# Kernel tuning notes

Measured on AMD Instinct MI355X. Metric: run time of the kernel, lower is better.

Reference implementation:

```python
import jax, jax.numpy as jnp
import numpy as np

BN_EPS = 1e-5

SOBEL_X = jnp.array([[-1., 0., 1.], [-2., 0., 2.], [-1., 0., 1.]], jnp.float32).reshape(1, 1, 3, 3)
SOBEL_Y = jnp.array([[-1., -2., -1.], [0., 0., 0.], [1., 2., 1.]], jnp.float32).reshape(1, 1, 3, 3)


def _conv2d(x, w, stride, pad):
    return jax.lax.conv_general_dilated(x, w, window_strides=(stride, stride),
                                        padding=((pad, pad), (pad, pad)),
                                        dimension_numbers=('NCHW', 'OIHW', 'NCHW'))


def _resize_bilinear_align_corners(x, H, W):
    # x: [b,c,h1,w1] -> [b,c,H,W], align_corners=True
    b, c, h1, w1 = x.shape
    ys = jnp.linspace(0., h1 - 1., H)
    xs = jnp.linspace(0., w1 - 1., W)
    y0 = jnp.floor(ys).astype(jnp.int32)
    x0 = jnp.floor(xs).astype(jnp.int32)
    y1 = jnp.minimum(y0 + 1, h1 - 1)
    x1 = jnp.minimum(x0 + 1, w1 - 1)
    wy = (ys - y0)[None, None, :, None]
    wx = (xs - x0)[None, None, None, :]
    top = x[:, :, y0, :]
    bot = x[:, :, y1, :]
    top = top[:, :, :, x0] * (1. - wx) + top[:, :, :, x1] * wx
    bot = bot[:, :, :, x0] * (1. - wx) + bot[:, :, :, x1] * wx
    return top * (1. - wy) + bot * wy


def setup_inputs() -> dict:
    key = jax.random.key(0)
    ks = jax.random.split(key, 6)
    b, c, h, w = 4, 64, 128, 128
    return {
        'x': jax.random.normal(ks[0], (b, c, h, w), jnp.float32),
        'conv_w': jax.random.normal(ks[1], (c, c, 3, 3), jnp.float32) * 0.05,
        'conv_b': jax.random.normal(ks[2], (c,), jnp.float32) * 0.05,
        'bn_gamma': jnp.ones((c,), jnp.float32),
        'bn_beta': jnp.zeros((c,), jnp.float32),
        'bn_mean': jnp.zeros((c,), jnp.float32),
        'bn_var': jnp.ones((c,), jnp.float32),
        'fc1_w': jax.random.normal(ks[3], (c, c), jnp.float32) * 0.1,
        'fc2_w': jax.random.normal(ks[4], (c, c), jnp.float32) * 0.1,
        'fc3_w': jax.random.normal(ks[5], (c, c), jnp.float32) * 0.1,
    }


def reference(x, conv_w, conv_b, bn_gamma, bn_beta, bn_mean, bn_var, fc1_w, fc2_w, fc3_w):
    b, c, h, w = x.shape
    # input block: conv s2 + BN (eval) + relu
    y = _conv2d(x, conv_w, 2, 1) + conv_b[None, :, None, None]
    y = (y - bn_mean[None, :, None, None]) * jax.lax.rsqrt(bn_var + BN_EPS)[None, :, None, None]
    y = jax.nn.relu(y * bn_gamma[None, :, None, None] + bn_beta[None, :, None, None])
    b, c, h1, w1 = y.shape
    N = h1 * w1
    # pre: [b,c,h1,w1] -> [b,1,N,c]
    xp = y.reshape(b, c, N).transpose(0, 2, 1).reshape(b, 1, N, c)
    # Sobel adjacency over the N "node" axis
    sx = jnp.abs(_conv2d(xp, SOBEL_X, 1, 1)).reshape(b, N, c)
    sy = jnp.abs(_conv2d(xp, SOBEL_Y, 1, 1)).reshape(b, N, c)
    A = jnp.einsum('bnc,bmc->bnm', sx, sy)  # [b,N,N]
    # torch nn.Softmax() (no dim) on a 3D tensor => legacy dim=0 (batch axis)
    A = jax.nn.softmax(A, axis=0)
    # normalize: D^-0.5 (A + I) D^-0.5, batched
    A1 = A + jnp.eye(N, dtype=A.dtype)[None]
    dinv = A1.sum(axis=2) ** -0.5  # [b,N]
    A = dinv[:, :, None] * A1 * dinv[:, None, :]
    # GCN propagation; Conv1d k=1 no-bias == channel matmul
    xg = xp.reshape(b, N, c)
    xg = jax.nn.relu(jnp.einsum('bnm,bmc,oc->bno', A, xg, fc1_w))
    xg = jax.nn.relu(jnp.einsum('bnm,bmc,oc->bno', A, xg, fc2_w))
    xg = jnp.einsum('bnm,bmc,oc->bon', A, xg, fc3_w)  # [b,c,N]
    out = xg.reshape(b, c, h1, w1)
    return _resize_bilinear_align_corners(out, h, w)
```

## Files before the change

kernel.cpp:

```cpp
#include <hip/hip_runtime.h>
#include <hip/hip_bf16.h>

typedef float f32x4 __attribute__((ext_vector_type(4)));
typedef short bf16x8 __attribute__((ext_vector_type(8)));

#define NB 4
#define NC 64
#define NH 128
#define NW 128
#define NN 4096
#define BN_EPS_C 1e-5f

__device__ __forceinline__ void gld16(const void* g, void* l) {
    __builtin_amdgcn_global_load_lds((const __attribute__((address_space(1))) void*)g,
                                     (__attribute__((address_space(3))) void*)l, 16, 0, 0);
}
__device__ __forceinline__ ushort pkbf(float f) {
    __hip_bfloat16 h = __float2bfloat16(f);
    return *(ushort*)&h;
}

__global__ __launch_bounds__(256) void k_conv(
    const float* __restrict__ x, const float* __restrict__ cw, const float* __restrict__ cb,
    const float* __restrict__ bng, const float* __restrict__ bnb, const float* __restrict__ bnm,
    const float* __restrict__ bnv, float* __restrict__ xg)
{
    int b = blockIdx.y, oh = blockIdx.x;
    int tid = threadIdx.x;
    int ow = tid & 63;
    int wg = __builtin_amdgcn_readfirstlane(tid >> 6);
    float acc[16];
#pragma unroll
    for (int j = 0; j < 16; ++j) acc[j] = 0.f;
    const float* xb = x + (size_t)b * NC * NH * NW;
    int ih0 = 2 * oh - 1;
    for (int ic = 0; ic < 64; ++ic) {
        const float* xr = xb + (size_t)ic * (NH * NW);
        float v00, v01, v02, v10, v11, v12, v20, v21, v22;
        if (ih0 < 0) { v00 = v01 = v02 = 0.f; }
        else {
            const float* p = xr + ih0 * NW + 2 * ow;
            float2 t = *(const float2*)p;
            v01 = t.x; v02 = t.y;
            v00 = (ow == 0) ? 0.f : p[-1];
        }
        { const float* p = xr + (ih0 + 1) * NW + 2 * ow; float2 t = *(const float2*)p; v11 = t.x; v12 = t.y; v10 = (ow == 0) ? 0.f : p[-1]; }
        { const float* p = xr + (ih0 + 2) * NW + 2 * ow; float2 t = *(const float2*)p; v21 = t.x; v22 = t.y; v20 = (ow == 0) ? 0.f : p[-1]; }
        const float* wp = cw + ((size_t)(wg * 16) * 64 + ic) * 9;
#pragma unroll
        for (int j = 0; j < 16; ++j) {
            const float* wj = wp + (size_t)j * 576;
            acc[j] += wj[0] * v00 + wj[1] * v01 + wj[2] * v02
                    + wj[3] * v10 + wj[4] * v11 + wj[5] * v12
                    + wj[6] * v20 + wj[7] * v21 + wj[8] * v22;
        }
    }
    int n = oh * 64 + ow;
    float* outr = xg + ((size_t)b * NN + n) * 64;
#pragma unroll
    for (int j = 0; j < 16; ++j) {
        int oc = wg * 16 + j;
        float s = bng[oc] * rsqrtf(bnv[oc] + BN_EPS_C);
        float y = (acc[j] + cb[oc] - bnm[oc]) * s + bnb[oc];
        outr[oc] = fmaxf(y, 0.f);
    }
}

__global__ __launch_bounds__(256) void k_sobel(
    const float* __restrict__ xg,
    __hip_bfloat16* __restrict__ xh, __hip_bfloat16* __restrict__ xl,
    __hip_bfloat16* __restrict__ yh, __hip_bfloat16* __restrict__ yl)
{
    __shared__ float t[66][66];
    int b = blockIdx.y;
    int n0 = blockIdx.x * 64;
    int tid = threadIdx.x;
    const float* xb = xg + (size_t)b * NN * 64;
    for (int idx = tid; idx < 66 * 64; idx += 256) {
        int r = idx >> 6, c = idx & 63;
        int n = n0 - 1 + r;
        float v = (n >= 0 && n < NN) ? xb[(size_t)n * 64 + c] : 0.f;
        t[r][c + 1] = v;
    }
    for (int idx = tid; idx < 66; idx += 256) { t[idx][0] = 0.f; t[idx][65] = 0.f; }
    __syncthreads();
    int c = tid & 63, rg = tid >> 6;
    int lc = c + 1;
    for (int i = 0; i < 16; ++i) {
        int r = rg * 16 + i;
        float tm1 = t[r][lc - 1],     t0 = t[r][lc],     tp1 = t[r][lc + 1];
        float mm1 = t[r + 1][lc - 1],                    mp1 = t[r + 1][lc + 1];
        float bm1 = t[r + 2][lc - 1], b0 = t[r + 2][lc], bp1 = t[r + 2][lc + 1];
        float gx = (tp1 + 2.f * mp1 + bp1) - (tm1 + 2.f * mm1 + bm1);
        float gy = (bm1 + 2.f * b0 + bp1) - (tm1 + 2.f * t0 + tp1);
        float ax = fabsf(gx), ay = fabsf(gy);
        size_t o = ((size_t)b * NN + n0 + r) * 64 + c;
        __hip_bfloat16 h1 = __float2bfloat16(ax);
        xh[o] = h1;
        xl[o] = __float2bfloat16(ax - __bfloat162float(h1));
        __hip_bfloat16 h2 = __float2bfloat16(ay);
        yh[o] = h2;
        yl[o] = __float2bfloat16(ay - __bfloat162float(h2));
    }
}

__global__ __launch_bounds__(256) void k_logits(
    const __hip_bfloat16* __restrict__ xh_, const __hip_bfloat16* __restrict__ xl_,
    const __hip_bfloat16* __restrict__ yh_, const __hip_bfloat16* __restrict__ yl_,
    __hip_bfloat16* __restrict__ A, float* __restrict__ rowsum)
{
    __shared__ __align__(16) ushort lds_u[24576];
    ushort* a_hi = lds_u;
    ushort* a_lo = lds_u + 4096;
    ushort* b_hi = lds_u + 8192;
    ushort* b_lo = lds_u + 16384;
    ushort* st   = lds_u;

    const ushort* xh = (const ushort*)xh_;
    const ushort* xl = (const ushort*)xl_;
    const ushort* yh = (const ushort*)yh_;
    const ushort* yl = (const ushort*)yl_;
    int tid = threadIdx.x, lane = tid & 63;
    int w = __builtin_amdgcn_readfirstlane(tid >> 6);
    int l15 = lane & 15, lg = lane >> 4;
    int wn = w >> 1, wm = w & 1;
    int m0 = blockIdx.x * 128, n0 = blockIdx.y * 64;

    f32x4 acc[4][2][4];
#pragma unroll
    for (int b = 0; b < 4; ++b)
#pragma unroll
        for (int t = 0; t < 2; ++t)
#pragma unroll
            for (int u = 0; u < 4; ++u) acc[b][t][u] = (f32x4){0.f, 0.f, 0.f, 0.f};

    for (int b = 0; b < 4; ++b) {
        if (b) __syncthreads();
#pragma unroll
        for (int p = 0; p < 2; ++p) {
            int ch = p * 256 + tid;
            int r = ch >> 3;
            int sc = ((ch & 7) ^ (r & 7)) * 8;
            gld16(xh + ((size_t)b * NN + n0 + r) * 64 + sc, (char*)a_hi + ch * 16);
            gld16(xl + ((size_t)b * NN + n0 + r) * 64 + sc, (char*)a_lo + ch * 16);
        }
#pragma unroll
        for (int p = 0; p < 4; ++p) {
            int ch = p * 256 + tid;
            int r = ch >> 3;
            int sc = ((ch & 7) ^ (r & 7)) * 8;
            gld16(yh + ((size_t)b * NN + m0 + r) * 64 + sc, (char*)b_hi + ch * 16);
            gld16(yl + ((size_t)b * NN + m0 + r) * 64 + sc, (char*)b_lo + ch * 16);
        }
        __syncthreads();
#pragma unroll
        for (int ks = 0; ks < 2; ++ks) {
            bf16x8 ah[2], al2[2], bh4[4], bl4[4];
#pragma unroll
            for (int t = 0; t < 2; ++t) {
                int r = wn * 32 + t * 16 + l15;
                int c16 = (ks * 4 + lg) ^ (r & 7);
                ah[t]  = *(const bf16x8*)((const char*)a_hi + r * 128 + c16 * 16);
                al2[t] = *(const bf16x8*)((const char*)a_lo + r * 128 + c16 * 16);
            }
#pragma unroll
            for (int u = 0; u < 4; ++u) {
                int r = wm * 64 + u * 16 + l15;
                int c16 = (ks * 4 + lg) ^ (r & 7);
                bh4[u] = *(const bf16x8*)((const char*)b_hi + r * 128 + c16 * 16);
                bl4[u] = *(const bf16x8*)((const char*)b_lo + r * 128 + c16 * 16);
            }
#pragma unroll
            for (int t = 0; t < 2; ++t)
#pragma unroll
                for (int u = 0; u < 4; ++u) {
                    f32x4 a = acc[b][t][u];
                    a = __builtin_amdgcn_mfma_f32_16x16x32_bf16(ah[t],  bh4[u], a, 0, 0, 0);
                    a = __builtin_amdgcn_mfma_f32_16x16x32_bf16(ah[t],  bl4[u], a, 0, 0, 0);
                    a = __builtin_amdgcn_mfma_f32_16x16x32_bf16(al2[t], bh4[u], a, 0, 0, 0);
                    acc[b][t][u] = a;
                }
        }
    }

    float rs[4][2][4];
#pragma unroll
    for (int b = 0; b < 4; ++b)
#pragma unroll
        for (int t = 0; t < 2; ++t)
#pragma unroll
            for (int j = 0; j < 4; ++j) rs[b][t][j] = 0.f;
#pragma unroll
    for (int t = 0; t < 2; ++t)
#pragma unroll
        for (int u = 0; u < 4; ++u)
#pragma unroll
            for (int j = 0; j < 4; ++j) {
                float v0 = acc[0][t][u][j], v1 = acc[1][t][u][j];
                float v2 = acc[2][t][u][j], v3 = acc[3][t][u][j];
                float mx = fmaxf(fmaxf(v0, v1), fmaxf(v2, v3));
                float e0 = __expf(v0 - mx), e1 = __expf(v1 - mx);
                float e2 = __expf(v2 - mx), e3 = __expf(v3 - mx);
                float rz = 1.f / (e0 + e1 + e2 + e3);
                acc[0][t][u][j] = e0 * rz; acc[1][t][u][j] = e1 * rz;
                acc[2][t][u][j] = e2 * rz; acc[3][t][u][j] = e3 * rz;
                rs[0][t][j] += e0 * rz; rs[1][t][j] += e1 * rz;
                rs[2][t][j] += e2 * rz; rs[3][t][j] += e3 * rz;
            }
#pragma unroll
    for (int b = 0; b < 4; ++b)
#pragma unroll
        for (int t = 0; t < 2; ++t)
#pragma unroll
            for (int j = 0; j < 4; ++j) {
                float s = rs[b][t][j];
                s += __shfl_xor(s, 1); s += __shfl_xor(s, 2);
                s += __shfl_xor(s, 4); s += __shfl_xor(s, 8);
                if (l15 == 0)
                    atomicAdd(&rowsum[(size_t)b * NN + n0 + wn * 32 + t * 16 + lg * 4 + j], s);
            }

#pragma unroll
    for (int b = 0; b < 4; ++b) {
        __syncthreads();
#pragma unroll
        for (int t = 0; t < 2; ++t)
#pragma unroll
            for (int u = 0; u < 4; ++u)
#pragma unroll
                for (int j = 0; j < 4; ++j) {
                    int row = wn * 32 + t * 16 + lg * 4 + j;
                    int col = wm * 64 + u * 16 + l15;
                    int c16 = (col >> 3) ^ (row & 7);
                    st[row * 128 + c16 * 8 + (col & 7)] = pkbf(acc[b][t][u][j]);
                }
        __syncthreads();
#pragma unroll
        for (int p = 0; p < 4; ++p) {
            int idx = p * 256 + tid;
            int row = idx >> 4, cl = idx & 15;
            int c16 = cl ^ (row & 7);
            bf16x8 v = *(const bf16x8*)(st + row * 128 + c16 * 8);
            *(bf16x8*)((ushort*)A + (size_t)b * NN * NN + (size_t)(n0 + row) * NN + m0 + cl * 8) = v;
        }
    }
}

__global__ __launch_bounds__(256) void k_dinv(const float* __restrict__ rs, float* __restrict__ dinv)
{
    int i = blockIdx.x * 256 + threadIdx.x;
    dinv[i] = rsqrtf(rs[i] + 1.0f);
}

__global__ __launch_bounds__(256) void k_small(
    const float* __restrict__ h, const float* __restrict__ fc, const float* __restrict__ dinv,
    __hip_bfloat16* __restrict__ tT, float* __restrict__ tf)
{
    int blk = blockIdx.x;
    int b = blk >> 6, m0 = (blk & 63) * 64;
    int tid = threadIdx.x;
    int mi = tid & 63, m = m0 + mi;
    int oq = __builtin_amdgcn_readfirstlane(tid >> 6);
    const float* hr = h + ((size_t)b * NN + m) * 64;
    float hv[64];
#pragma unroll
    for (int i = 0; i < 16; ++i) {
        float4 v = *(const float4*)(hr + 4 * i);
        hv[4 * i] = v.x; hv[4 * i + 1] = v.y; hv[4 * i + 2] = v.z; hv[4 * i + 3] = v.w;
    }
    float dv = dinv[(size_t)b * NN + m];
#pragma unroll
    for (int j = 0; j < 16; ++j) {
        int o = oq * 16 + j;
        const float* wr = fc + (size_t)o * 64;
        float a = 0.f;
#pragma unroll
        for (int c2 = 0; c2 < 64; ++c2) a += hv[c2] * wr[c2];
        a *= dv;
        tf[((size_t)b * NN + m) * 64 + o] = a;
        tT[((size_t)b * 64 + o) * NN + m] = __float2bfloat16(a);
    }
}

__global__ __launch_bounds__(256) void k_big(
    const __hip_bfloat16* __restrict__ A_, const __hip_bfloat16* __restrict__ tT_,
    float* __restrict__ part)
{
    __shared__ __align__(16) ushort ab[2][4096];
    const ushort* A = (const ushort*)A_;
    const ushort* tT = (const ushort*)tT_;
    int blk = blockIdx.x;
    int ntile = blk & 63, b = (blk >> 6) & 3, ks = blk >> 8;
    int n0 = ntile * 64;
    int tid = threadIdx.x, lane = tid & 63;
    int w = __builtin_amdgcn_readfirstlane(tid >> 6);
    int l15 = lane & 15, lg = lane >> 4;
    size_t kw0 = (size_t)ks * 1024;
    const ushort* Ab = A + (size_t)b * NN * NN;
    const ushort* Tb = tT + ((size_t)b * 64 + w * 16 + l15) * NN + kw0;

    f32x4 acc[4];
#pragma unroll
    for (int ti = 0; ti < 4; ++ti) acc[ti] = (f32x4){0.f, 0.f, 0.f, 0.f};

#define STAGE(buf, s) do { \
    _Pragma("unroll") \
    for (int p = 0; p < 2; ++p) { \
        int ch = p * 256 + tid; \
        int r = ch >> 3; \
        int sc = ((ch & 7) ^ (r & 7)) * 8; \
        gld16(Ab + (size_t)(n0 + r) * NN + kw0 + (size_t)(s) * 64 + sc, (char*)ab[buf] + ch * 16); \
    } \
} while (0)

    STAGE(0, 0);
    bf16x8 bf0 = *(const bf16x8*)(Tb + lg * 8);
    bf16x8 bf1 = *(const bf16x8*)(Tb + 32 + lg * 8);
    bf16x8 nf0 = bf0, nf1 = bf1;
    __syncthreads();

    int cur = 0;
    for (int s = 0; s < 16; ++s) {
        if (s < 15) {
            STAGE(cur ^ 1, s + 1);
            nf0 = *(const bf16x8*)(Tb + (size_t)(s + 1) * 64 + lg * 8);
            nf1 = *(const bf16x8*)(Tb + (size_t)(s + 1) * 64 + 32 + lg * 8);
        }
#pragma unroll
        for (int kc = 0; kc < 2; ++kc) {
            bf16x8 bfr = (kc == 0) ? bf0 : bf1;
#pragma unroll
            for (int ti = 0; ti < 4; ++ti) {
                int r = ti * 16 + l15;
                int c16 = (kc * 4 + lg) ^ (r & 7);
                bf16x8 afr = *(const bf16x8*)((const char*)ab[cur] + r * 128 + c16 * 16);
                acc[ti] = __builtin_amdgcn_mfma_f32_16x16x32_bf16(afr, bfr, acc[ti], 0, 0, 0);
            }
        }
        bf0 = nf0; bf1 = nf1;
        __syncthreads();
        cur ^= 1;
    }
#undef STAGE

    float* pp = part + ((size_t)(ks * 4 + b) * NN + n0) * 64;
#pragma unroll
    for (int ti = 0; ti < 4; ++ti)
#pragma unroll
        for (int j = 0; j < 4; ++j)
            pp[(size_t)(ti * 16 + lg * 4 + j) * 64 + w * 16 + l15] = acc[ti][j];
}

__global__ __launch_bounds__(256) void k_red(
    const float* __restrict__ part, const float* __restrict__ tf, const float* __restrict__ dinv,
    float* __restrict__ outp, int relu)
{
    int v = blockIdx.x * 256 + threadIdx.x;
    size_t e0 = (size_t)v * 4;
    int b = (int)(e0 >> 18);
    int n = (int)((e0 >> 6) & (NN - 1));
    f32x4 u = (f32x4){0.f, 0.f, 0.f, 0.f};
#pragma unroll
    for (int s = 0; s < 4; ++s)
        u += *(const f32x4*)(part + (size_t)s * (4 * (size_t)NN * 64) + e0);
    f32x4 t = *(const f32x4*)(tf + e0);
    float dn = dinv[(size_t)b * NN + n];
    f32x4 r;
#pragma unroll
    for (int j = 0; j < 4; ++j) {
        float vv = dn * (u[j] + t[j]);
        if (relu) vv = fmaxf(vv, 0.f);
        r[j] = vv;
    }
    *(f32x4*)(outp + e0) = r;
}

__global__ __launch_bounds__(256) void k_up(const float* __restrict__ o3, float* __restrict__ outp)
{
    int b = blockIdx.y, Y = blockIdx.x;
    int tid = threadIdx.x;
    int X = tid & 127, cg = tid >> 7;
    int iy = Y * 63; int y0 = iy / 127; float wy = (float)(iy - y0 * 127) * (1.f / 127.f);
    int y1 = min(y0 + 1, 63);
    int ix = X * 63; int x0 = ix / 127; float wx = (float)(ix - x0 * 127) * (1.f / 127.f);
    int x1 = min(x0 + 1, 63);
    const float* p00 = o3 + ((size_t)b * NN + y0 * 64 + x0) * 64;
    const float* p01 = o3 + ((size_t)b * NN + y0 * 64 + x1) * 64;
    const float* p10 = o3 + ((size_t)b * NN + y1 * 64 + x0) * 64;
    const float* p11 = o3 + ((size_t)b * NN + y1 * 64 + x1) * 64;
    float w00 = (1.f - wy) * (1.f - wx), w01 = (1.f - wy) * wx;
    float w10 = wy * (1.f - wx), w11 = wy * wx;
#pragma unroll
    for (int j = 0; j < 32; ++j) {
        int ch = cg * 32 + j;
        float v = w00 * p00[ch] + w01 * p01[ch] + w10 * p10[ch] + w11 * p11[ch];
        outp[(((size_t)b * 64 + ch) * 128 + Y) * 128 + X] = v;
    }
}

extern "C" void kernel_launch(void* const* d_in, const int* in_sizes, int n_in,
                              void* d_out, int out_size, void* d_ws, size_t ws_size,
                              hipStream_t stream)
{
    const float* x   = (const float*)d_in[0];
    const float* cw  = (const float*)d_in[1];
    const float* cb  = (const float*)d_in[2];
    const float* bng = (const float*)d_in[3];
    const float* bnb = (const float*)d_in[4];
    const float* bnm = (const float*)d_in[5];
    const float* bnv = (const float*)d_in[6];
    const float* fc1 = (const float*)d_in[7];
    const float* fc2 = (const float*)d_in[8];
    const float* fc3 = (const float*)d_in[9];
    float* outp = (float*)d_out;

    char* ws = (char*)d_ws;
    size_t off = 0;
    auto alloc = [&](size_t bytes) -> void* {
        void* p = ws + off;
        off += (bytes + 255) & ~(size_t)255;
        return p;
    };
    __hip_bfloat16* Abuf = (__hip_bfloat16*)alloc((size_t)NB * NN * NN * 2);
    float* part   = (float*)alloc((size_t)4 * NB * NN * 64 * 4);
    float* xg     = (float*)alloc((size_t)NB * NN * 64 * 4);
    __hip_bfloat16* sxh = (__hip_bfloat16*)alloc((size_t)NB * NN * 64 * 2);
    __hip_bfloat16* sxl = (__hip_bfloat16*)alloc((size_t)NB * NN * 64 * 2);
    __hip_bfloat16* syh = (__hip_bfloat16*)alloc((size_t)NB * NN * 64 * 2);
    __hip_bfloat16* syl = (__hip_bfloat16*)alloc((size_t)NB * NN * 64 * 2);
    __hip_bfloat16* tT = (__hip_bfloat16*)alloc((size_t)NB * 64 * NN * 2);
    float* tf     = (float*)alloc((size_t)NB * NN * 64 * 4);
    float* h1     = (float*)alloc((size_t)NB * NN * 64 * 4);
    float* h2     = (float*)alloc((size_t)NB * NN * 64 * 4);
    float* o3     = (float*)alloc((size_t)NB * NN * 64 * 4);
    float* rowsum = (float*)alloc((size_t)NB * NN * 4);
    float* dinvb  = (float*)alloc((size_t)NB * NN * 4);

    hipMemsetAsync(rowsum, 0, (size_t)NB * NN * 4, stream);

    k_conv<<<dim3(64, 4), 256, 0, stream>>>(x, cw, cb, bng, bnb, bnm, bnv, xg);
    k_sobel<<<dim3(64, 4), 256, 0, stream>>>(xg, sxh, sxl, syh, syl);
    k_logits<<<dim3(32, 64), 256, 0, stream>>>(sxh, sxl, syh, syl, Abuf, rowsum);
    k_dinv<<<64, 256, 0, stream>>>(rowsum, dinvb);

    k_small<<<256, 256, 0, stream>>>(xg, fc1, dinvb, tT, tf);
    k_big<<<1024, 256, 0, stream>>>(Abuf, tT, part);
    k_red<<<1024, 256, 0, stream>>>(part, tf, dinvb, h1, 1);

    k_small<<<256, 256, 0, stream>>>(h1, fc2, dinvb, tT, tf);
    k_big<<<1024, 256, 0, stream>>>(Abuf, tT, part);
    k_red<<<1024, 256, 0, stream>>>(part, tf, dinvb, h2, 1);

    k_small<<<256, 256, 0, stream>>>(h2, fc3, dinvb, tT, tf);
    k_big<<<1024, 256, 0, stream>>>(Abuf, tT, part);
    k_red<<<1024, 256, 0, stream>>>(part, tf, dinvb, o3, 0);

    k_up<<<dim3(128, 4), 256, 0, stream>>>(o3, outp);
}
```

Baseline: 470.8 us.

## Double-buffer logits GEMM staging, load Y fragments to registers, store A directly

```diff
diff --git a/kernel.cpp b/kernel.cpp
--- a/kernel.cpp
+++ b/kernel.cpp
@@ -15,9 +15,9 @@
     __builtin_amdgcn_global_load_lds((const __attribute__((address_space(1))) void*)g,
                                      (__attribute__((address_space(3))) void*)l, 16, 0, 0);
 }
-__device__ __forceinline__ ushort pkbf(float f) {
-    __hip_bfloat16 h = __float2bfloat16(f);
-    return *(ushort*)&h;
+__device__ __forceinline__ unsigned pk2(float a, float b) {
+    __hip_bfloat16 x = __float2bfloat16(a), y = __float2bfloat16(b);
+    return (unsigned)*(unsigned short*)&x | ((unsigned)*(unsigned short*)&y << 16);
 }
 
 __global__ __launch_bounds__(256) void k_conv(
@@ -104,26 +104,19 @@
     }
 }
 
-__global__ __launch_bounds__(256) void k_logits(
+__global__ __launch_bounds__(256, 2) void k_logits(
     const __hip_bfloat16* __restrict__ xh_, const __hip_bfloat16* __restrict__ xl_,
     const __hip_bfloat16* __restrict__ yh_, const __hip_bfloat16* __restrict__ yl_,
     __hip_bfloat16* __restrict__ A, float* __restrict__ rowsum)
 {
-    __shared__ __align__(16) ushort lds_u[24576];
-    ushort* a_hi = lds_u;
-    ushort* a_lo = lds_u + 4096;
-    ushort* b_hi = lds_u + 8192;
-    ushort* b_lo = lds_u + 16384;
-    ushort* st   = lds_u;
-
+    __shared__ __align__(16) ushort xs[2][2][4096];
     const ushort* xh = (const ushort*)xh_;
     const ushort* xl = (const ushort*)xl_;
     const ushort* yh = (const ushort*)yh_;
     const ushort* yl = (const ushort*)yl_;
     int tid = threadIdx.x, lane = tid & 63;
-    int w = __builtin_amdgcn_readfirstlane(tid >> 6);
+    int wv = __builtin_amdgcn_readfirstlane(tid >> 6);
     int l15 = lane & 15, lg = lane >> 4;
-    int wn = w >> 1, wm = w & 1;
     int m0 = blockIdx.x * 128, n0 = blockIdx.y * 64;
 
     f32x4 acc[4][2][4];
@@ -134,66 +127,77 @@
 #pragma unroll
             for (int u = 0; u < 4; ++u) acc[b][t][u] = (f32x4){0.f, 0.f, 0.f, 0.f};
 
-    for (int b = 0; b < 4; ++b) {
-        if (b) __syncthreads();
-#pragma unroll
-        for (int p = 0; p < 2; ++p) {
-            int ch = p * 256 + tid;
-            int r = ch >> 3;
-            int sc = ((ch & 7) ^ (r & 7)) * 8;
-            gld16(xh + ((size_t)b * NN + n0 + r) * 64 + sc, (char*)a_hi + ch * 16);
-            gld16(xl + ((size_t)b * NN + n0 + r) * 64 + sc, (char*)a_lo + ch * 16);
-        }
-#pragma unroll
-        for (int p = 0; p < 4; ++p) {
-            int ch = p * 256 + tid;
-            int r = ch >> 3;
-            int sc = ((ch & 7) ^ (r & 7)) * 8;
-            gld16(yh + ((size_t)b * NN + m0 + r) * 64 + sc, (char*)b_hi + ch * 16);
-            gld16(yl + ((size_t)b * NN + m0 + r) * 64 + sc, (char*)b_lo + ch * 16);
-        }
-        __syncthreads();
-#pragma unroll
-        for (int ks = 0; ks < 2; ++ks) {
-            bf16x8 ah[2], al2[2], bh4[4], bl4[4];
-#pragma unroll
-            for (int t = 0; t < 2; ++t) {
-                int r = wn * 32 + t * 16 + l15;
-                int c16 = (ks * 4 + lg) ^ (r & 7);
-                ah[t]  = *(const bf16x8*)((const char*)a_hi + r * 128 + c16 * 16);
-                al2[t] = *(const bf16x8*)((const char*)a_lo + r * 128 + c16 * 16);
-            }
-#pragma unroll
-            for (int u = 0; u < 4; ++u) {
-                int r = wm * 64 + u * 16 + l15;
-                int c16 = (ks * 4 + lg) ^ (r & 7);
-                bh4[u] = *(const bf16x8*)((const char*)b_hi + r * 128 + c16 * 16);
-                bl4[u] = *(const bf16x8*)((const char*)b_lo + r * 128 + c16 * 16);
-            }
-#pragma unroll
-            for (int t = 0; t < 2; ++t)
-#pragma unroll
-                for (int u = 0; u < 4; ++u) {
-                    f32x4 a = acc[b][t][u];
-                    a = __builtin_amdgcn_mfma_f32_16x16x32_bf16(ah[t],  bh4[u], a, 0, 0, 0);
-                    a = __builtin_amdgcn_mfma_f32_16x16x32_bf16(ah[t],  bl4[u], a, 0, 0, 0);
-                    a = __builtin_amdgcn_mfma_f32_16x16x32_bf16(al2[t], bh4[u], a, 0, 0, 0);
-                    acc[b][t][u] = a;
-                }
-        }
-    }
-
-    float rs[4][2][4];
+#define STAGEX(buf, b_) do { \
+    _Pragma("unroll") \
+    for (int p = 0; p < 2; ++p) { \
+        int ch = p * 256 + tid; \
+        int r = ch >> 3; \
+        int sc = ((ch & 7) ^ (r & 7)) * 8; \
+        gld16(xh + ((size_t)(b_) * NN + n0 + r) * 64 + sc, (char*)xs[buf][0] + ch * 16); \
+        gld16(xl + ((size_t)(b_) * NN + n0 + r) * 64 + sc, (char*)xs[buf][1] + ch * 16); \
+    } \
+} while (0)
+
+#define YLOAD(Y, b_) do { \
+    _Pragma("unroll") \
+    for (int t = 0; t < 2; ++t) { \
+        size_t rb = ((size_t)(b_) * NN + m0 + wv * 32 + t * 16 + l15) * 64 + lg * 8; \
+        Y[t][0][0] = *(const bf16x8*)(yh + rb); \
+        Y[t][1][0] = *(const bf16x8*)(yh + rb + 32); \
+        Y[t][0][1] = *(const bf16x8*)(yl + rb); \
+        Y[t][1][1] = *(const bf16x8*)(yl + rb + 32); \
+    } \
+} while (0)
+
+#define COMPUTE(buf, Y, b_) do { \
+    _Pragma("unroll") \
+    for (int ks = 0; ks < 2; ++ks) { \
+        bf16x8 xf[4][2]; \
+        _Pragma("unroll") \
+        for (int u = 0; u < 4; ++u) { \
+            int r = u * 16 + l15; \
+            int c16 = (ks * 4 + lg) ^ (r & 7); \
+            xf[u][0] = *(const bf16x8*)((const char*)xs[buf][0] + r * 128 + c16 * 16); \
+            xf[u][1] = *(const bf16x8*)((const char*)xs[buf][1] + r * 128 + c16 * 16); \
+        } \
+        _Pragma("unroll") \
+        for (int t = 0; t < 2; ++t) \
+            _Pragma("unroll") \
+            for (int u = 0; u < 4; ++u) { \
+                f32x4 a = acc[b_][t][u]; \
+                a = __builtin_amdgcn_mfma_f32_16x16x32_bf16(Y[t][ks][0], xf[u][0], a, 0, 0, 0); \
+                a = __builtin_amdgcn_mfma_f32_16x16x32_bf16(Y[t][ks][0], xf[u][1], a, 0, 0, 0); \
+                a = __builtin_amdgcn_mfma_f32_16x16x32_bf16(Y[t][ks][1], xf[u][0], a, 0, 0, 0); \
+                acc[b_][t][u] = a; \
+            } \
+    } \
+} while (0)
+
+    bf16x8 yA[2][2][2], yB[2][2][2];
+    STAGEX(0, 0); YLOAD(yA, 0);
+    __syncthreads();
+    STAGEX(1, 1); YLOAD(yB, 1); COMPUTE(0, yA, 0);
+    __syncthreads();
+    STAGEX(0, 2); YLOAD(yA, 2); COMPUTE(1, yB, 1);
+    __syncthreads();
+    STAGEX(1, 3); YLOAD(yB, 3); COMPUTE(0, yA, 2);
+    __syncthreads();
+    COMPUTE(1, yB, 3);
+#undef STAGEX
+#undef YLOAD
+#undef COMPUTE
+
+    float rsum[4][4];
 #pragma unroll
     for (int b = 0; b < 4; ++b)
 #pragma unroll
-        for (int t = 0; t < 2; ++t)
-#pragma unroll
-            for (int j = 0; j < 4; ++j) rs[b][t][j] = 0.f;
+        for (int u = 0; u < 4; ++u) rsum[b][u] = 0.f;
+
 #pragma unroll
     for (int t = 0; t < 2; ++t)
 #pragma unroll
-        for (int u = 0; u < 4; ++u)
+        for (int u = 0; u < 4; ++u) {
+            float av[4][4];
 #pragma unroll
             for (int j = 0; j < 4; ++j) {
                 float v0 = acc[0][t][u][j], v1 = acc[1][t][u][j];
@@ -202,48 +206,32 @@
                 float e0 = __expf(v0 - mx), e1 = __expf(v1 - mx);
                 float e2 = __expf(v2 - mx), e3 = __expf(v3 - mx);
                 float rz = 1.f / (e0 + e1 + e2 + e3);
-                acc[0][t][u][j] = e0 * rz; acc[1][t][u][j] = e1 * rz;
-                acc[2][t][u][j] = e2 * rz; acc[3][t][u][j] = e3 * rz;
-                rs[0][t][j] += e0 * rz; rs[1][t][j] += e1 * rz;
-                rs[2][t][j] += e2 * rz; rs[3][t][j] += e3 * rz;
+                av[0][j] = e0 * rz; av[1][j] = e1 * rz;
+                av[2][j] = e2 * rz; av[3][j] = e3 * rz;
+                rsum[0][u] += av[0][j]; rsum[1][u] += av[1][j];
+                rsum[2][u] += av[2][j]; rsum[3][u] += av[3][j];
             }
+            int n = n0 + u * 16 + l15;
+            int m = m0 + wv * 32 + t * 16 + lg * 4;
+#pragma unroll
+            for (int b = 0; b < 4; ++b) {
+                uint2 pv;
+                pv.x = pk2(av[b][0], av[b][1]);
+                pv.y = pk2(av[b][2], av[b][3]);
+                *(uint2*)((ushort*)A + (size_t)b * NN * NN + (size_t)n * NN + m) = pv;
+            }
+        }
+
 #pragma unroll
     for (int b = 0; b < 4; ++b)
 #pragma unroll
-        for (int t = 0; t < 2; ++t)
-#pragma unroll
-            for (int j = 0; j < 4; ++j) {
-                float s = rs[b][t][j];
-                s += __shfl_xor(s, 1); s += __shfl_xor(s, 2);
-                s += __shfl_xor(s, 4); s += __shfl_xor(s, 8);
-                if (l15 == 0)
-                    atomicAdd(&rowsum[(size_t)b * NN + n0 + wn * 32 + t * 16 + lg * 4 + j], s);
-            }
-
-#pragma unroll
-    for (int b = 0; b < 4; ++b) {
-        __syncthreads();
-#pragma unroll
-        for (int t = 0; t < 2; ++t)
-#pragma unroll
-            for (int u = 0; u < 4; ++u)
-#pragma unroll
-                for (int j = 0; j < 4; ++j) {
-                    int row = wn * 32 + t * 16 + lg * 4 + j;
-                    int col = wm * 64 + u * 16 + l15;
-                    int c16 = (col >> 3) ^ (row & 7);
-                    st[row * 128 + c16 * 8 + (col & 7)] = pkbf(acc[b][t][u][j]);
-                }
-        __syncthreads();
-#pragma unroll
-        for (int p = 0; p < 4; ++p) {
-            int idx = p * 256 + tid;
-            int row = idx >> 4, cl = idx & 15;
-            int c16 = cl ^ (row & 7);
-            bf16x8 v = *(const bf16x8*)(st + row * 128 + c16 * 8);
-            *(bf16x8*)((ushort*)A + (size_t)b * NN * NN + (size_t)(n0 + row) * NN + m0 + cl * 8) = v;
-        }
-    }
+        for (int u = 0; u < 4; ++u) {
+            float s = rsum[b][u];
+            s += __shfl_xor(s, 16);
+            s += __shfl_xor(s, 32);
+            if (lane < 16)
+                atomicAdd(&rowsum[(size_t)b * NN + n0 + u * 16 + l15], s);
+        }
 }
 
 __global__ __launch_bounds__(256) void k_dinv(const float* __restrict__ rs, float* __restrict__ dinv)
```

Measured after the change: 408.4 us. 13.3% less time.
